# Optimization experiments

Hardware: AMD Instinct MI355X
Metric: run time of the kernel (lower is better)

## Reference

```python
import jax, jax.numpy as jnp
import numpy as np

TAU = 0.1            # tau_instance == tau_proto == tau_guidance
ALPHA_RES = 0.2
LOGIT_SCALE = 5.0
K_NEI = 5
N_WAYS = 20
N_SHOTS = 5


def l2n(x):
    return x / jnp.maximum(jnp.linalg.norm(x, axis=-1, keepdims=True), 1e-12)


def sparse_adj(f, k, tau):
    # sim: [B, n, n]; keep only top-k per row, softmax over them
    sim = jnp.einsum('bnd,bmd->bnm', f, f)
    vals, idx = jax.lax.top_k(sim, k)
    B, n, _ = sim.shape
    mask = jnp.full_like(sim, -jnp.inf)
    bi = jnp.arange(B)[:, None, None]
    ri = jnp.arange(n)[None, :, None]
    mask = mask.at[bi, ri, idx].set(vals)
    return jax.nn.softmax(mask / tau, axis=-1)


def gnn_layer(x, adj, W, b, s):
    # message passing + linear + tanh + scaled residual (dropout=0 / eval)
    msg = jnp.einsum('bnm,bmd->bnd', adj, x)
    upd = jnp.tanh(msg @ W.T + b)
    return x + s * upd


def setup_inputs() -> dict:
    key = jax.random.key(0)
    ks = jax.random.split(key, 10)
    B, N, K, Q, D, L = 256, N_WAYS, N_SHOTS, 75, 512, 4
    NT = N * K + Q
    xav = 1.0 / np.sqrt(D)
    return {
        'V_feat': jax.random.normal(ks[0], (B, NT, D), jnp.float32),
        'P_feat': jax.random.normal(ks[1], (B, N, D), jnp.float32),
        'query_y': jax.random.randint(ks[2], (B, Q), 0, N),
        'igb_W': jax.random.normal(ks[3], (L, D, D), jnp.float32) * xav,
        'igb_b': jnp.zeros((L, D), jnp.float32),
        'igb_scale': jax.random.normal(ks[4], (L,), jnp.float32) * 0.1,
        'pgb_W': jax.random.normal(ks[5], (L, D, D), jnp.float32) * xav,
        'pgb_b': jnp.zeros((L, D), jnp.float32),
        'pgb_scale': jax.random.normal(ks[6], (L,), jnp.float32) * 0.1,
        'alpha': jax.random.uniform(ks[7], (), jnp.float32),
        'beta': jax.random.uniform(ks[8], (), jnp.float32),
    }


def reference(V_feat, P_feat, query_y, igb_W, igb_b, igb_scale,
              pgb_W, pgb_b, pgb_scale, alpha, beta):
    B, NT, D = V_feat.shape
    N, K = N_WAYS, N_SHOTS
    NK = N * K
    Q = NT - NK
    L = igb_W.shape[0]

    V = l2n(V_feat)
    P = l2n(P_feat)
    V0, P0 = V, P

    yl = query_y.reshape(B * Q)
    total = jnp.float32(0.0)
    final_logits = None
    for i in range(L):
        # instance graph branch
        adj_I = sparse_adj(V, K_NEI, TAU)
        V = gnn_layer(V, adj_I, igb_W[i], igb_b[i], igb_scale[i])
        V = l2n((1.0 - ALPHA_RES) * V + ALPHA_RES * V0)
        # prototype graph branch
        adj_P = sparse_adj(P, min(K_NEI, N), TAU)
        P = gnn_layer(P, adj_P, pgb_W[i], pgb_b[i], pgb_scale[i])
        P = l2n((1.0 - ALPHA_RES) * P + ALPHA_RES * P0)
        # visual class centers and adapted prototypes
        VC = l2n(V[:, :NK, :].reshape(B, N, K, D).mean(axis=2))
        Pa = l2n(alpha * P + (1.0 - alpha) * VC)
        # cross-modal softmax guidance
        sims = jnp.einsum('bnd,bmd->bnm', V, Pa)
        soft = jax.nn.softmax(sims / TAU, axis=-1)
        guide = jnp.einsum('bnm,bmd->bnd', soft, Pa)
        V = l2n(beta * V + (1.0 - beta) * guide)
        # per-step logits and CE loss (label_smoothing = 0)
        logits = LOGIT_SCALE * jnp.einsum('bqd,bnd->bqn', V[:, NK:, :], Pa)
        lf = logits.reshape(B * Q, N)
        ce = jnp.mean(jax.nn.logsumexp(lf, axis=-1)
                      - jnp.take_along_axis(lf, yl[:, None], axis=1)[:, 0])
        total = total + ce
        final_logits = logits

    loss = total / L
    pred = jnp.argmax(final_logits.reshape(B * Q, N), axis=-1)
    acc = jnp.mean((pred == yl).astype(jnp.float32))
    return (loss, acc)
```

## Files before the change

kernel.cpp:

```cpp
#include <hip/hip_runtime.h>
#include <math.h>

#define B_EP 256
#define NT 175
#define NWAYS 20
#define KSHOT 5
#define NKS 100
#define NQ 75
#define DIM 512
#define NLAYERS 4
#define TAU_INV 10.0f
#define LOGIT_SCALE 5.0f
#define KNEI 5
#define SIMLD 176
#define STLD2 72
#define PALD 520
#define NVB 700

typedef unsigned int u32;
typedef unsigned short u16;
typedef __attribute__((ext_vector_type(8))) short s16x8;
typedef __attribute__((ext_vector_type(4))) float f32x4;

__device__ __forceinline__ float waveReduceSum(float v) {
#pragma unroll
  for (int off = 32; off >= 1; off >>= 1) v += __shfl_xor(v, off);
  return v;
}

__device__ __forceinline__ u32 pack2bf(float a, float b) {
  u32 ua = __float_as_uint(a), ub = __float_as_uint(b);
  ua = (ua + 0x7FFFu + ((ua >> 16) & 1u)) >> 16;
  ub = (ub + 0x7FFFu + ((ub >> 16) & 1u)) >> 16;
  return ua | (ub << 16);
}

__device__ __forceinline__ u16 pack1bf(float a) {
  u32 ua = __float_as_uint(a);
  return (u16)((ua + 0x7FFFu + ((ua >> 16) & 1u)) >> 16);
}

__device__ __forceinline__ float bflo(u32 u) { return __uint_as_float(u << 16); }
__device__ __forceinline__ float bfhi(u32 u) { return __uint_as_float(u & 0xFFFF0000u); }
__device__ __forceinline__ float bf1(u16 h) { return __uint_as_float((u32)h << 16); }

__device__ __forceinline__ float tanh_fast(float x) {
  float e = __expf(2.f * x);
  return 1.f - 2.f * __builtin_amdgcn_rcpf(e + 1.f);
}

__device__ __forceinline__ s16x8 ldfrag(const u16* p) {
  return __builtin_bit_cast(s16x8, *(const uint4*)p);
}

__device__ __forceinline__ void gload16(const u16* g, u16* l) {
  __builtin_amdgcn_global_load_lds(
      (const __attribute__((address_space(1))) void*)g,
      (__attribute__((address_space(3))) void*)l, 16, 0, 0);
}

__global__ void init_accum_kernel(float* acc) {
  if (threadIdx.x < 16) acc[threadIdx.x] = 0.f;
}

__global__ void cvt_bf16_kernel(const float* __restrict__ in1,
                                const float* __restrict__ in2,
                                u16* __restrict__ outb, int n8_each) {
  const int nb1 = (n8_each + 255) / 256;
  int bid = blockIdx.x;
  const float* in = (bid < nb1) ? in1 : in2;
  u16* out = (bid < nb1) ? outb : outb + (size_t)n8_each * 8;
  if (bid >= nb1) bid -= nb1;
  int t = bid * 256 + threadIdx.x;
  if (t >= n8_each) return;
  const float4* p = (const float4*)(in + (size_t)t * 8);
  float4 a = p[0], b = p[1];
  uint4 r;
  r.x = pack2bf(a.x, a.y);
  r.y = pack2bf(a.z, a.w);
  r.z = pack2bf(b.x, b.y);
  r.w = pack2bf(b.z, b.w);
  *(uint4*)(out + (size_t)t * 8) = r;
}

__global__ void l2n_init_kernel(const float* __restrict__ in,
                                u16* __restrict__ outb,
                                u16* __restrict__ out0b) {
  const size_t row = blockIdx.x;
  const int lane = threadIdx.x;
  const float* src = in + row * DIM;
  float4 a = *(const float4*)(src + 4 * lane);
  float4 b = *(const float4*)(src + 256 + 4 * lane);
  float ss = a.x * a.x + a.y * a.y + a.z * a.z + a.w * a.w +
             b.x * b.x + b.y * b.y + b.z * b.z + b.w * b.w;
  ss = waveReduceSum(ss);
  const float inv = 1.f / fmaxf(sqrtf(ss), 1e-12f);
  a.x *= inv; a.y *= inv; a.z *= inv; a.w *= inv;
  b.x *= inv; b.y *= inv; b.z *= inv; b.w *= inv;
  uint2 pa, pb;
  pa.x = pack2bf(a.x, a.y); pa.y = pack2bf(a.z, a.w);
  pb.x = pack2bf(b.x, b.y); pb.y = pack2bf(b.z, b.w);
  *(uint2*)(outb + row * DIM + 4 * lane) = pa;
  *(uint2*)(outb + row * DIM + 256 + 4 * lane) = pb;
  *(uint2*)(out0b + row * DIM + 4 * lane) = pa;
  *(uint2*)(out0b + row * DIM + 256 + 4 * lane) = pb;
}

__global__ __launch_bounds__(256) void graph_front_kernel(
    const u16* __restrict__ VB, const u16* __restrict__ PB,
    u16* __restrict__ MSGB, u16* __restrict__ PMSGB) {
  const int p = blockIdx.x;
  const int tid = threadIdx.x;
  const int wave = tid >> 6, lane = tid & 63;
  __shared__ __align__(16) u16 smem[25088];
  __shared__ float Gl2[NWAYS][NWAYS];
  __shared__ float Wl2[NWAYS][KNEI];
  __shared__ int Il2[NWAYS][KNEI];
  if (p < 3 * B_EP) {
    const int b = p & 255, sl = p >> 8;
    u16* SIMs = smem;
    u16* Vst = smem + 64 * SIMLD;
    const u16* Vb = VB + (size_t)b * NT * DIM;
    for (int i = tid; i < (192 - NT) * STLD2; i += 256)
      Vst[NT * STLD2 + i] = 0;
    f32x4 acc[4][4];
#pragma unroll
    for (int m = 0; m < 4; ++m)
#pragma unroll
      for (int n = 0; n < 4; ++n) acc[m][n] = (f32x4){0.f, 0.f, 0.f, 0.f};
    const int part = lane >> 4;
    for (int kk = 0; kk < DIM; kk += 64) {
      __syncthreads();
#pragma unroll
      for (int r6 = 0; r6 < 6; ++r6) {
        const int idx = tid + 256 * r6;
        if (idx < NT * 8) {
          const int row = idx >> 3, pp = idx & 7;
          uint4 v = *(const uint4*)(Vb + (size_t)row * DIM + kk + pp * 8);
          *(uint4*)&Vst[row * STLD2 + pp * 8] = v;
        }
      }
      __syncthreads();
      if (wave < 3) {
#pragma unroll
        for (int ks = 0; ks < 2; ++ks) {
          s16x8 fa[4], fb[4];
#pragma unroll
          for (int m = 0; m < 4; ++m)
            fa[m] = ldfrag(&Vst[(sl * 64 + m * 16 + (lane & 15)) * STLD2 +
                                ks * 32 + part * 8]);
#pragma unroll
          for (int n = 0; n < 4; ++n)
            fb[n] = ldfrag(&Vst[(wave * 64 + n * 16 + (lane & 15)) * STLD2 +
                                ks * 32 + part * 8]);
#pragma unroll
          for (int m = 0; m < 4; ++m)
#pragma unroll
            for (int n = 0; n < 4; ++n)
              acc[m][n] = __builtin_amdgcn_mfma_f32_16x16x32_bf16(
                  fa[m], fb[n], acc[m][n], 0, 0, 0);
        }
      }
    }
    const int r_ = (lane >> 4) * 4, c_ = lane & 15;
    if (wave < 3) {
#pragma unroll
      for (int m = 0; m < 4; ++m)
#pragma unroll
        for (int n = 0; n < 4; ++n)
#pragma unroll
          for (int j = 0; j < 4; ++j) {
            const int rl = m * 16 + r_ + j;
            const int c = wave * 64 + n * 16 + c_;
            if (sl * 64 + rl < NT && c < NT)
              SIMs[rl * SIMLD + c] = pack1bf(acc[m][n][j]);
          }
    }
    __syncthreads();
    for (int rl = wave; rl < 64; rl += 4) {
      const int rg = sl * 64 + rl;
      if (rg >= NT) break;
      u32 pk[3];
#pragma unroll
      for (int t = 0; t < 3; ++t) {
        int j = lane + 64 * t;
        if (j < NT) {
          u32 v = SIMs[rl * SIMLD + j];
          u32 key = v ^ ((v >> 15) ? 0xFFFFu : 0x8000u);
          pk[t] = (key << 8) | (u32)(255 - j);
        } else {
          pk[t] = 0u;
        }
      }
      float topv[KNEI];
      int topi[KNEI];
#pragma unroll
      for (int t = 0; t < KNEI; ++t) {
        u32 c = max(pk[0], max(pk[1], pk[2]));
#pragma unroll
        for (int off = 32; off >= 1; off >>= 1)
          c = max(c, (u32)__shfl_xor((int)c, off));
#pragma unroll
        for (int u = 0; u < 3; ++u)
          if (pk[u] == c) pk[u] = 0u;
        const u32 k16 = (c >> 8) & 0xFFFFu;
        const u32 v16 = (k16 & 0x8000u) ? (k16 ^ 0x8000u) : (~k16 & 0xFFFFu);
        topv[t] = bf1((u16)v16);
        topi[t] = 255 - (int)(c & 0xFFu);
      }
      float w[KNEI];
      float wsum = 0.f;
#pragma unroll
      for (int t = 0; t < KNEI; ++t) {
        w[t] = __expf((topv[t] - topv[0]) * TAU_INV);
        wsum += w[t];
      }
      const float invs = 1.f / wsum;
      float a8[8] = {0.f, 0.f, 0.f, 0.f, 0.f, 0.f, 0.f, 0.f};
#pragma unroll
      for (int t = 0; t < KNEI; ++t) {
        uint4 v = *(const uint4*)(Vb + (size_t)topi[t] * DIM + 8 * lane);
        a8[0] += w[t] * bflo(v.x); a8[1] += w[t] * bfhi(v.x);
        a8[2] += w[t] * bflo(v.y); a8[3] += w[t] * bfhi(v.y);
        a8[4] += w[t] * bflo(v.z); a8[5] += w[t] * bfhi(v.z);
        a8[6] += w[t] * bflo(v.w); a8[7] += w[t] * bfhi(v.w);
      }
      uint4 r;
      r.x = pack2bf(a8[0] * invs, a8[1] * invs);
      r.y = pack2bf(a8[2] * invs, a8[3] * invs);
      r.z = pack2bf(a8[4] * invs, a8[5] * invs);
      r.w = pack2bf(a8[6] * invs, a8[7] * invs);
      *(uint4*)(MSGB + ((size_t)b * NT + rg) * DIM + 8 * lane) = r;
    }
  } else {
    const int b = p - 3 * B_EP;
    u16* Pl = smem;
    const u16* Pb = PB + (size_t)b * NWAYS * DIM;
    for (int c = tid; c < 32 * 64; c += 256) {
      int m = c >> 6, ko = (c & 63) * 8;
      uint4 v = {0, 0, 0, 0};
      if (m < NWAYS) v = *(const uint4*)(Pb + (size_t)m * DIM + ko);
      *(uint4*)&Pl[m * PALD + ko] = v;
    }
    __syncthreads();
    if (wave == 0) {
      f32x4 acc[2][2];
#pragma unroll
      for (int m = 0; m < 2; ++m)
#pragma unroll
        for (int n = 0; n < 2; ++n) acc[m][n] = (f32x4){0.f, 0.f, 0.f, 0.f};
      for (int kk = 0; kk < DIM; kk += 32) {
        s16x8 f[2];
#pragma unroll
        for (int m = 0; m < 2; ++m)
          f[m] = ldfrag(&Pl[(m * 16 + (lane & 15)) * PALD + kk +
                            (lane >> 4) * 8]);
#pragma unroll
        for (int m = 0; m < 2; ++m)
#pragma unroll
          for (int n = 0; n < 2; ++n)
            acc[m][n] = __builtin_amdgcn_mfma_f32_16x16x32_bf16(
                f[m], f[n], acc[m][n], 0, 0, 0);
      }
      const int r_ = (lane >> 4) * 4, c_ = lane & 15;
#pragma unroll
      for (int m = 0; m < 2; ++m)
#pragma unroll
        for (int n = 0; n < 2; ++n)
#pragma unroll
          for (int j = 0; j < 4; ++j) {
            int r = m * 16 + r_ + j, c = n * 16 + c_;
            if (r < NWAYS && c < NWAYS) Gl2[r][c] = acc[m][n][j];
          }
    }
    __syncthreads();
    if (tid < NWAYS) {
      float sims[NWAYS];
#pragma unroll
      for (int m = 0; m < NWAYS; ++m) sims[m] = Gl2[tid][m];
      float topv[KNEI];
      int topi[KNEI];
#pragma unroll
      for (int t = 0; t < KNEI; ++t) {
        float bv = -INFINITY;
        int bi = 0;
#pragma unroll
        for (int m = 0; m < NWAYS; ++m)
          if (sims[m] > bv) { bv = sims[m]; bi = m; }
        sims[bi] = -INFINITY;
        topv[t] = bv;
        topi[t] = bi;
      }
      float w[KNEI], wsum = 0.f;
#pragma unroll
      for (int t = 0; t < KNEI; ++t) {
        w[t] = __expf((topv[t] - topv[0]) * TAU_INV);
        wsum += w[t];
      }
      const float invs = 1.f / wsum;
#pragma unroll
      for (int t = 0; t < KNEI; ++t) {
        Wl2[tid][t] = w[t] * invs;
        Il2[tid][t] = topi[t];
      }
    }
    __syncthreads();
    u16* outp = PMSGB + (size_t)b * NWAYS * DIM;
    for (int n = wave; n < NWAYS; n += 4) {
      float a8[8] = {0.f, 0.f, 0.f, 0.f, 0.f, 0.f, 0.f, 0.f};
#pragma unroll
      for (int t = 0; t < KNEI; ++t) {
        const float w = Wl2[n][t];
        uint4 v = *(const uint4*)&Pl[Il2[n][t] * PALD + 8 * lane];
        a8[0] += w * bflo(v.x); a8[1] += w * bfhi(v.x);
        a8[2] += w * bflo(v.y); a8[3] += w * bfhi(v.y);
        a8[4] += w * bflo(v.z); a8[5] += w * bfhi(v.z);
        a8[6] += w * bflo(v.w); a8[7] += w * bfhi(v.w);
      }
      uint4 r;
      r.x = pack2bf(a8[0], a8[1]);
      r.y = pack2bf(a8[2], a8[3]);
      r.z = pack2bf(a8[4], a8[5]);
      r.w = pack2bf(a8[6], a8[7]);
      *(uint4*)(outp + (size_t)n * DIM + 8 * lane) = r;
    }
  }
}

__global__ __launch_bounds__(512) void gemm_fused_kernel(
    const u16* __restrict__ Av, const u16* __restrict__ Ap,
    const u16* __restrict__ Wv, const u16* __restrict__ Wp,
    const float* __restrict__ bias_v, const float* __restrict__ bias_p,
    const float* __restrict__ sv, const float* __restrict__ sp,
    u16* __restrict__ XBv, u16* __restrict__ XBp,
    const u16* __restrict__ X0v, const u16* __restrict__ X0p) {
  const int bid = blockIdx.x;
  const bool isV = bid < NVB;
  const int row0 = (isV ? bid : bid - NVB) * 64;
  const u16* A = isV ? Av : Ap;
  const u16* W = isV ? Wv : Wp;
  const float* bias = isV ? bias_v : bias_p;
  const float* scale_ptr = isV ? sv : sp;
  u16* XB = isV ? XBv : XBp;
  const u16* X0B = isV ? X0v : X0p;
  const int tid = threadIdx.x, wave = tid >> 6, lane = tid & 63;
  __shared__ __align__(16) u16 smem[18432];
  u16* Bs = smem;
  u16* As = smem + 16384;
  f32x4 acc[4][4];
#pragma unroll
  for (int m = 0; m < 4; ++m)
#pragma unroll
    for (int n = 0; n < 4; ++n) acc[m][n] = (f32x4){0.f, 0.f, 0.f, 0.f};
  const int rsrc = lane >> 2;
  const int ksrc = (lane & 3) * 8;
  for (int kk = 0; kk < DIM; kk += 32) {
#pragma unroll
    for (int q = 0; q < 4; ++q) {
      const int t = wave * 4 + q;
      gload16(W + (size_t)(t * 16 + rsrc) * DIM + kk + ksrc, Bs + t * 512);
    }
    if (wave < 4)
      gload16(A + (size_t)(row0 + wave * 16 + rsrc) * DIM + kk + ksrc,
              As + wave * 512);
    __syncthreads();
    s16x8 fa[4], fb[4];
#pragma unroll
    for (int m = 0; m < 4; ++m)
      fa[m] = ldfrag(&As[(m * 16 + (lane & 15)) * 32 + (lane >> 4) * 8]);
#pragma unroll
    for (int n = 0; n < 4; ++n)
      fb[n] = ldfrag(
          &Bs[(wave * 64 + n * 16 + (lane & 15)) * 32 + (lane >> 4) * 8]);
#pragma unroll
    for (int m = 0; m < 4; ++m)
#pragma unroll
      for (int n = 0; n < 4; ++n)
        acc[m][n] = __builtin_amdgcn_mfma_f32_16x16x32_bf16(fa[m], fb[n],
                                                            acc[m][n], 0, 0, 0);
    __syncthreads();
  }
  const float s = *scale_ptr;
  const int rq = lane >> 4, c_ = lane & 15;
  const int prow = tid >> 4, sub = tid & 15;
  const int rq2 = ((prow >> 2) & 3) << 1;
#pragma unroll
  for (int half = 0; half < 2; ++half) {
    __syncthreads();
#pragma unroll
    for (int n = 0; n < 4; ++n) {
      const int col = wave * 64 + n * 16 + c_;
      const float bc = bias[col];
      const int cbase = col >> 3, wof = col & 7;
#pragma unroll
      for (int mm = 0; mm < 2; ++mm) {
        const int m = half * 2 + mm;
#pragma unroll
        for (int j = 0; j < 4; ++j) {
          const int lr = mm * 16 + rq * 4 + j;
          const int cS = cbase ^ (((lr >> 2) & 3) << 1);
          smem[lr * 512 + cS * 8 + wof] =
              pack1bf(s * tanh_fast(acc[m][n][j] + bc));
        }
      }
    }
    __syncthreads();
    const int grow = row0 + half * 32 + prow;
    const u16* xrow = XB + (size_t)grow * DIM;
    const u16* x0row = X0B + (size_t)grow * DIM;
    float ss = 0.f;
#pragma unroll
    for (int i = 0; i < 4; ++i) {
      const int c = sub + 16 * i;
      uint4 xb = *(const uint4*)(xrow + c * 8);
      uint4 x0 = *(const uint4*)(x0row + c * 8);
      uint4 uu = *(const uint4*)&smem[prow * 512 + (c ^ rq2) * 8];
      float t0 = 0.8f * (bflo(xb.x) + bflo(uu.x)) + 0.2f * bflo(x0.x);
      float t1 = 0.8f * (bfhi(xb.x) + bfhi(uu.x)) + 0.2f * bfhi(x0.x);
      float t2 = 0.8f * (bflo(xb.y) + bflo(uu.y)) + 0.2f * bflo(x0.y);
      float t3 = 0.8f * (bfhi(xb.y) + bfhi(uu.y)) + 0.2f * bfhi(x0.y);
      float t4 = 0.8f * (bflo(xb.z) + bflo(uu.z)) + 0.2f * bflo(x0.z);
      float t5 = 0.8f * (bfhi(xb.z) + bfhi(uu.z)) + 0.2f * bfhi(x0.z);
      float t6 = 0.8f * (bflo(xb.w) + bflo(uu.w)) + 0.2f * bflo(x0.w);
      float t7 = 0.8f * (bfhi(xb.w) + bfhi(uu.w)) + 0.2f * bfhi(x0.w);
      ss += t0 * t0 + t1 * t1 + t2 * t2 + t3 * t3 + t4 * t4 + t5 * t5 +
            t6 * t6 + t7 * t7;
      uint4 tp;
      tp.x = pack2bf(t0, t1); tp.y = pack2bf(t2, t3);
      tp.z = pack2bf(t4, t5); tp.w = pack2bf(t6, t7);
      *(uint4*)&smem[prow * 512 + (c ^ rq2) * 8] = tp;
    }
#pragma unroll
    for (int off = 8; off >= 1; off >>= 1) ss += __shfl_xor(ss, off, 16);
    const float inv = 1.f / fmaxf(sqrtf(ss), 1e-12f);
    u16* orow = XB + (size_t)grow * DIM;
#pragma unroll
    for (int i = 0; i < 4; ++i) {
      const int c = sub + 16 * i;
      uint4 tp = *(const uint4*)&smem[prow * 512 + (c ^ rq2) * 8];
      uint4 r;
      r.x = pack2bf(bflo(tp.x) * inv, bfhi(tp.x) * inv);
      r.y = pack2bf(bflo(tp.y) * inv, bfhi(tp.y) * inv);
      r.z = pack2bf(bflo(tp.z) * inv, bfhi(tp.z) * inv);
      r.w = pack2bf(bflo(tp.w) * inv, bfhi(tp.w) * inv);
      *(uint4*)(orow + c * 8) = r;
    }
  }
}

__global__ __launch_bounds__(512) void episode_post_kernel(
    u16* __restrict__ VB, const u16* __restrict__ PB,
    const int* __restrict__ qy, const float* __restrict__ alpha_ptr,
    const float* __restrict__ beta_ptr, float* __restrict__ accum,
    int is_last) {
  const int p = blockIdx.x;
  const int b = p & 255, sl = p >> 8;
  const int tid = threadIdx.x, wave = tid >> 6, lane = tid & 63;
  __shared__ __align__(16) u16 palds[NWAYS * PALD];
  __shared__ float SIMSl[96 * NWAYS];
  __shared__ float Gl[NWAYS][NWAYS + 1];
  __shared__ float red[16];
  const u16* Vb0 = VB + (size_t)b * NT * DIM;
  const float alpha = *alpha_ptr, oma = 1.f - alpha;
  const float beta = *beta_ptr, omb = 1.f - beta;
  const int row_lo = sl * 96;
  const int row_hi = (row_lo + 96 < NT) ? (row_lo + 96) : NT;
  for (int n = wave; n < NWAYS; n += 8) {
    const u16* base = Vb0 + (size_t)n * KSHOT * DIM;
    float a8[8] = {0.f, 0.f, 0.f, 0.f, 0.f, 0.f, 0.f, 0.f};
#pragma unroll
    for (int k = 0; k < KSHOT; ++k) {
      uint4 v = *(const uint4*)(base + (size_t)k * DIM + 8 * lane);
      a8[0] += bflo(v.x); a8[1] += bfhi(v.x);
      a8[2] += bflo(v.y); a8[3] += bfhi(v.y);
      a8[4] += bflo(v.z); a8[5] += bfhi(v.z);
      a8[6] += bflo(v.w); a8[7] += bfhi(v.w);
    }
    float ss = 0.f;
#pragma unroll
    for (int t = 0; t < 8; ++t) ss += a8[t] * a8[t];
    ss = waveReduceSum(ss);
    const float inv = 1.f / fmaxf(sqrtf(ss), 1e-12f);
    {
      uint4 pp = *(const uint4*)(PB + ((size_t)b * NWAYS + n) * DIM + 8 * lane);
      a8[0] = alpha * bflo(pp.x) + oma * a8[0] * inv;
      a8[1] = alpha * bfhi(pp.x) + oma * a8[1] * inv;
      a8[2] = alpha * bflo(pp.y) + oma * a8[2] * inv;
      a8[3] = alpha * bfhi(pp.y) + oma * a8[3] * inv;
      a8[4] = alpha * bflo(pp.z) + oma * a8[4] * inv;
      a8[5] = alpha * bfhi(pp.z) + oma * a8[5] * inv;
      a8[6] = alpha * bflo(pp.w) + oma * a8[6] * inv;
      a8[7] = alpha * bfhi(pp.w) + oma * a8[7] * inv;
    }
    float s2 = 0.f;
#pragma unroll
    for (int t = 0; t < 8; ++t) s2 += a8[t] * a8[t];
    s2 = waveReduceSum(s2);
    const float inv2 = 1.f / fmaxf(sqrtf(s2), 1e-12f);
    uint4 r;
    r.x = pack2bf(a8[0] * inv2, a8[1] * inv2);
    r.y = pack2bf(a8[2] * inv2, a8[3] * inv2);
    r.z = pack2bf(a8[4] * inv2, a8[5] * inv2);
    r.w = pack2bf(a8[6] * inv2, a8[7] * inv2);
    *(uint4*)&palds[n * PALD + 8 * lane] = r;
  }
  __syncthreads();
  if (wave < 4) {
    const int r0w = (wave < 3) ? (row_lo + wave * 32) : NT;
    f32x4 sacc[2][2];
#pragma unroll
    for (int m = 0; m < 2; ++m)
#pragma unroll
      for (int n = 0; n < 2; ++n) sacc[m][n] = (f32x4){0.f, 0.f, 0.f, 0.f};
    const int part = lane >> 4, fr = lane & 15;
    for (int kk = 0; kk < DIM; kk += 32) {
      s16x8 fa[2], fb[2];
#pragma unroll
      for (int m = 0; m < 2; ++m) {
        const int row = r0w + m * 16 + fr;
        if (row < NT) {
          fa[m] = __builtin_bit_cast(
              s16x8, *(const uint4*)(Vb0 + (size_t)row * DIM + kk + part * 8));
        } else {
          int pr = row - NT;
          if (pr > NWAYS - 1) pr = NWAYS - 1;
          fa[m] = ldfrag(&palds[pr * PALD + kk + part * 8]);
        }
      }
#pragma unroll
      for (int n = 0; n < 2; ++n)
        fb[n] = ldfrag(&palds[(n * 16 + fr) * PALD + kk + part * 8]);
#pragma unroll
      for (int m = 0; m < 2; ++m)
#pragma unroll
        for (int n = 0; n < 2; ++n)
          sacc[m][n] = __builtin_amdgcn_mfma_f32_16x16x32_bf16(
              fa[m], fb[n], sacc[m][n], 0, 0, 0);
    }
    const int r_ = (lane >> 4) * 4, c_ = lane & 15;
#pragma unroll
    for (int m = 0; m < 2; ++m)
#pragma unroll
      for (int n = 0; n < 2; ++n)
#pragma unroll
        for (int j = 0; j < 4; ++j) {
          const int r = r0w + m * 16 + r_ + j, c = n * 16 + c_;
          if (c >= NWAYS) continue;
          if (r >= row_lo && r < row_hi && wave < 3)
            SIMSl[(r - row_lo) * NWAYS + c] = sacc[m][n][j];
          else if (r >= NT && r < NT + NWAYS)
            Gl[r - NT][c] = sacc[m][n][j];
        }
  }
  __syncthreads();
  float ce_acc = 0.f, ac_acc = 0.f;
  if (!(is_last && sl == 0)) {
    const int rs = is_last ? ((row_lo > NKS ? row_lo : NKS) + wave)
                           : (row_lo + wave);
    for (int row = rs; row < row_hi; row += 8) {
      float s[NWAYS];
#pragma unroll
      for (int m = 0; m < NWAYS; ++m)
        s[m] = SIMSl[(row - row_lo) * NWAYS + m];
      float mx = s[0];
#pragma unroll
      for (int m = 1; m < NWAYS; ++m) mx = fmaxf(mx, s[m]);
      float e[NWAYS], wsum = 0.f, dN = 0.f;
#pragma unroll
      for (int m = 0; m < NWAYS; ++m) {
        e[m] = __expf((s[m] - mx) * TAU_INV);
        wsum += e[m];
        dN += e[m] * s[m];
      }
      const float cg = omb / wsum;
      const int ln = lane & 31;
      float sg = 0.f;
      if (ln < NWAYS) {
#pragma unroll
        for (int m = 0; m < NWAYS; ++m) sg += e[m] * Gl[m][ln];
      }
      float ege = (ln < NWAYS) ? e[ln] * sg : 0.f;
#pragma unroll
      for (int off = 16; off >= 1; off >>= 1) ege += __shfl_xor(ege, off, 32);
      const float nn2 = beta * beta + 2.f * beta * cg * dN + cg * cg * ege;
      const float inv = 1.f / fmaxf(sqrtf(nn2), 1e-12f);
      if (!is_last) {
        u16* vrow = VB + ((size_t)b * NT + row) * DIM;
        uint4 v4 = *(const uint4*)(vrow + 8 * lane);
        float t0 = 0.f, t1 = 0.f, t2 = 0.f, t3 = 0.f;
        float t4 = 0.f, t5 = 0.f, t6 = 0.f, t7 = 0.f;
#pragma unroll
        for (int m = 0; m < NWAYS; ++m) {
          uint4 pp = *(const uint4*)&palds[m * PALD + 8 * lane];
          t0 += e[m] * bflo(pp.x); t1 += e[m] * bfhi(pp.x);
          t2 += e[m] * bflo(pp.y); t3 += e[m] * bfhi(pp.y);
          t4 += e[m] * bflo(pp.z); t5 += e[m] * bfhi(pp.z);
          t6 += e[m] * bflo(pp.w); t7 += e[m] * bfhi(pp.w);
        }
        uint4 r;
        r.x = pack2bf((beta * bflo(v4.x) + cg * t0) * inv,
                      (beta * bfhi(v4.x) + cg * t1) * inv);
        r.y = pack2bf((beta * bflo(v4.y) + cg * t2) * inv,
                      (beta * bfhi(v4.y) + cg * t3) * inv);
        r.z = pack2bf((beta * bflo(v4.z) + cg * t4) * inv,
                      (beta * bfhi(v4.z) + cg * t5) * inv);
        r.w = pack2bf((beta * bflo(v4.w) + cg * t6) * inv,
                      (beta * bfhi(v4.w) + cg * t7) * inv);
        *(uint4*)(vrow + 8 * lane) = r;
      }
      if (row >= NKS) {
        float l = (ln < NWAYS)
                      ? LOGIT_SCALE * inv * (beta * s[ln] + cg * sg)
                      : -1e30f;
        float bv = l;
        int bi = ln;
#pragma unroll
        for (int off = 16; off >= 1; off >>= 1) {
          float ov = __shfl_xor(bv, off, 32);
          int oi = __shfl_xor(bi, off, 32);
          if (ov > bv || (ov == bv && oi < bi)) { bv = ov; bi = oi; }
        }
        float se = (ln < NWAYS) ? __expf(l - bv) : 0.f;
#pragma unroll
        for (int off = 16; off >= 1; off >>= 1) se += __shfl_xor(se, off, 32);
        const int yt = qy[b * NQ + (row - NKS)];
        const float ly = __shfl(l, yt, 32);
        if (lane == 0) {
          ce_acc += bv + __logf(se) - ly;
          ac_acc += (bi == yt) ? 1.f : 0.f;
        }
      }
    }
  }
  if (lane == 0) {
    red[wave] = ce_acc;
    red[8 + wave] = ac_acc;
  }
  __syncthreads();
  if (tid == 0 && sl == 1) {
    float ce = 0.f, ac = 0.f;
#pragma unroll
    for (int w8 = 0; w8 < 8; ++w8) {
      ce += red[w8];
      ac += red[8 + w8];
    }
    atomicAdd(&accum[0], ce);
    if (is_last) atomicAdd(&accum[1], ac);
  } else if (tid == 0 && sl == 0 && !is_last) {
    float ce = 0.f;
#pragma unroll
    for (int w8 = 0; w8 < 8; ++w8) ce += red[w8];
    atomicAdd(&accum[0], ce);
  }
}

__global__ void finalize_kernel(const float* __restrict__ acc,
                                float* __restrict__ out) {
  out[0] = acc[0] / (float)(NLAYERS * B_EP * NQ);
  out[1] = acc[1] / (float)(B_EP * NQ);
}

extern "C" void kernel_launch(void* const* d_in, const int* in_sizes, int n_in,
                              void* d_out, int out_size, void* d_ws,
                              size_t ws_size, hipStream_t stream) {
  const float* V_feat = (const float*)d_in[0];
  const float* P_feat = (const float*)d_in[1];
  const int* query_y = (const int*)d_in[2];
  const float* igb_W = (const float*)d_in[3];
  const float* igb_b = (const float*)d_in[4];
  const float* igb_s = (const float*)d_in[5];
  const float* pgb_W = (const float*)d_in[6];
  const float* pgb_b = (const float*)d_in[7];
  const float* pgb_s = (const float*)d_in[8];
  const float* alpha = (const float*)d_in[9];
  const float* beta = (const float*)d_in[10];
  float* out = (float*)d_out;

  float* ws = (float*)d_ws;
  const size_t vsz = (size_t)B_EP * NT * DIM;
  const size_t psz = (size_t)B_EP * NWAYS * DIM;
  const size_t wsz = (size_t)NLAYERS * DIM * DIM;
  float* ACC = ws;
  u16* VB = (u16*)(ws + 16);
  u16* V0B = VB + vsz;
  u16* MSGB = V0B + vsz;
  u16* PB = MSGB + vsz;
  u16* P0B = PB + psz;
  u16* PMSGB = P0B + psz;
  u16* WB = PMSGB + psz;
  u16* WPB = WB + wsz;

  init_accum_kernel<<<1, 64, 0, stream>>>(ACC);
  l2n_init_kernel<<<B_EP * NT, 64, 0, stream>>>(V_feat, VB, V0B);
  l2n_init_kernel<<<B_EP * NWAYS, 64, 0, stream>>>(P_feat, PB, P0B);
  {
    const int n8 = (int)(wsz / 8);
    const int nb1 = (n8 + 255) / 256;
    cvt_bf16_kernel<<<2 * nb1, 256, 0, stream>>>(igb_W, pgb_W, WB, n8);
  }

  for (int i = 0; i < NLAYERS; ++i) {
    graph_front_kernel<<<4 * B_EP, 256, 0, stream>>>(VB, PB, MSGB, PMSGB);
    gemm_fused_kernel<<<NVB + B_EP * NWAYS / 64, 512, 0, stream>>>(
        MSGB, PMSGB, WB + (size_t)i * DIM * DIM, WPB + (size_t)i * DIM * DIM,
        igb_b + (size_t)i * DIM, pgb_b + (size_t)i * DIM, igb_s + i, pgb_s + i,
        VB, PB, V0B, P0B);
    episode_post_kernel<<<2 * B_EP, 512, 0, stream>>>(
        VB, PB, query_y, alpha, beta, ACC, (i == NLAYERS - 1) ? 1 : 0);
  }
  finalize_kernel<<<1, 1, 0, stream>>>(ACC, out);
}
```

Baseline: 768.5 us.

## Compute guidance update soft@Pa with MFMA using split-bf16 weights

```diff
diff --git a/kernel.cpp b/kernel.cpp
--- a/kernel.cpp
+++ b/kernel.cpp
@@ -15,6 +15,8 @@
 #define SIMLD 176
 #define STLD2 72
 #define PALD 520
+#define PTLD 32
+#define ELD 64
 #define NVB 700
 
 typedef unsigned int u32;
@@ -457,14 +459,18 @@
   const int b = p & 255, sl = p >> 8;
   const int tid = threadIdx.x, wave = tid >> 6, lane = tid & 63;
   __shared__ __align__(16) u16 palds[NWAYS * PALD];
+  __shared__ __align__(16) u16 PaT[512 * PTLD];
+  __shared__ __align__(16) u16 El[96 * ELD];
   __shared__ float SIMSl[96 * NWAYS];
   __shared__ float Gl[NWAYS][NWAYS + 1];
+  __shared__ float rowscal[96][2];
   __shared__ float red[16];
   const u16* Vb0 = VB + (size_t)b * NT * DIM;
   const float alpha = *alpha_ptr, oma = 1.f - alpha;
   const float beta = *beta_ptr, omb = 1.f - beta;
   const int row_lo = sl * 96;
   const int row_hi = (row_lo + 96 < NT) ? (row_lo + 96) : NT;
+  const int nrows = row_hi - row_lo;
   for (int n = wave; n < NWAYS; n += 8) {
     const u16* base = Vb0 + (size_t)n * KSHOT * DIM;
     float a8[8] = {0.f, 0.f, 0.f, 0.f, 0.f, 0.f, 0.f, 0.f};
@@ -497,12 +503,24 @@
     for (int t = 0; t < 8; ++t) s2 += a8[t] * a8[t];
     s2 = waveReduceSum(s2);
     const float inv2 = 1.f / fmaxf(sqrtf(s2), 1e-12f);
+    u16 h[8];
+#pragma unroll
+    for (int t = 0; t < 8; ++t) h[t] = pack1bf(a8[t] * inv2);
     uint4 r;
-    r.x = pack2bf(a8[0] * inv2, a8[1] * inv2);
-    r.y = pack2bf(a8[2] * inv2, a8[3] * inv2);
-    r.z = pack2bf(a8[4] * inv2, a8[5] * inv2);
-    r.w = pack2bf(a8[6] * inv2, a8[7] * inv2);
+    r.x = (u32)h[0] | ((u32)h[1] << 16);
+    r.y = (u32)h[2] | ((u32)h[3] << 16);
+    r.z = (u32)h[4] | ((u32)h[5] << 16);
+    r.w = (u32)h[6] | ((u32)h[7] << 16);
     *(uint4*)&palds[n * PALD + 8 * lane] = r;
+    if (!is_last) {
+#pragma unroll
+      for (int t = 0; t < 8; ++t)
+        PaT[(8 * lane + t) * PTLD + n] = h[t];
+    }
+  }
+  if (!is_last) {
+#pragma unroll
+    for (int z = 0; z < 12; ++z) PaT[tid * PTLD + NWAYS + z] = 0;
   }
   __syncthreads();
   if (wave < 4) {
@@ -552,6 +570,10 @@
             Gl[r - NT][c] = sacc[m][n][j];
         }
   }
+  if (!is_last) {
+    for (int i = tid; i < (96 - nrows) * ELD; i += 512)
+      El[nrows * ELD + i] = 0;
+  }
   __syncthreads();
   float ce_acc = 0.f, ac_acc = 0.f;
   if (!(is_last && sl == 0)) {
@@ -585,28 +607,17 @@
       const float nn2 = beta * beta + 2.f * beta * cg * dN + cg * cg * ege;
       const float inv = 1.f / fmaxf(sqrtf(nn2), 1e-12f);
       if (!is_last) {
-        u16* vrow = VB + ((size_t)b * NT + row) * DIM;
-        uint4 v4 = *(const uint4*)(vrow + 8 * lane);
-        float t0 = 0.f, t1 = 0.f, t2 = 0.f, t3 = 0.f;
-        float t4 = 0.f, t5 = 0.f, t6 = 0.f, t7 = 0.f;
-#pragma unroll
-        for (int m = 0; m < NWAYS; ++m) {
-          uint4 pp = *(const uint4*)&palds[m * PALD + 8 * lane];
-          t0 += e[m] * bflo(pp.x); t1 += e[m] * bfhi(pp.x);
-          t2 += e[m] * bflo(pp.y); t3 += e[m] * bfhi(pp.y);
-          t4 += e[m] * bflo(pp.z); t5 += e[m] * bfhi(pp.z);
-          t6 += e[m] * bflo(pp.w); t7 += e[m] * bfhi(pp.w);
-        }
-        uint4 r;
-        r.x = pack2bf((beta * bflo(v4.x) + cg * t0) * inv,
-                      (beta * bfhi(v4.x) + cg * t1) * inv);
-        r.y = pack2bf((beta * bflo(v4.y) + cg * t2) * inv,
-                      (beta * bfhi(v4.y) + cg * t3) * inv);
-        r.z = pack2bf((beta * bflo(v4.z) + cg * t4) * inv,
-                      (beta * bfhi(v4.z) + cg * t5) * inv);
-        r.w = pack2bf((beta * bflo(v4.w) + cg * t6) * inv,
-                      (beta * bfhi(v4.w) + cg * t7) * inv);
-        *(uint4*)(vrow + 8 * lane) = r;
+        u16 hi = 0, lo = 0;
+        if (ln < NWAYS) {
+          hi = pack1bf(e[ln]);
+          lo = pack1bf(e[ln] - bf1(hi));
+        }
+        El[(row - row_lo) * ELD + ln] = hi;
+        El[(row - row_lo) * ELD + 32 + ln] = lo;
+        if (lane == 0) {
+          rowscal[row - row_lo][0] = beta * inv;
+          rowscal[row - row_lo][1] = cg * inv;
+        }
       }
       if (row >= NKS) {
         float l = (ln < NWAYS)
@@ -637,6 +648,33 @@
     red[8 + wave] = ac_acc;
   }
   __syncthreads();
+  if (!is_last) {
+    const int tr = row_lo + wave * 16;
+    if (tr < row_hi) {
+      const int fr = lane & 15, part = lane >> 4;
+      const int er = (tr - row_lo + fr) * ELD + part * 8;
+      const s16x8 fahi = ldfrag(&El[er]);
+      const s16x8 falo = ldfrag(&El[er + 32]);
+      u16* vb = VB + ((size_t)b * NT) * DIM;
+      for (int t = 0; t < 32; ++t) {
+        const s16x8 fb = ldfrag(&PaT[(t * 16 + fr) * PTLD + part * 8]);
+        f32x4 acc = (f32x4){0.f, 0.f, 0.f, 0.f};
+        acc = __builtin_amdgcn_mfma_f32_16x16x32_bf16(fahi, fb, acc, 0, 0, 0);
+        acc = __builtin_amdgcn_mfma_f32_16x16x32_bf16(falo, fb, acc, 0, 0, 0);
+        const int gc = t * 16 + fr;
+#pragma unroll
+        for (int j = 0; j < 4; ++j) {
+          const int gr = tr + part * 4 + j;
+          if (gr < row_hi) {
+            const float bi_ = rowscal[gr - row_lo][0];
+            const float cgi = rowscal[gr - row_lo][1];
+            u16* vp = vb + (size_t)gr * DIM + gc;
+            *vp = pack1bf(bi_ * bf1(*vp) + cgi * acc[j]);
+          }
+        }
+      }
+    }
+  }
   if (tid == 0 && sl == 1) {
     float ce = 0.f, ac = 0.f;
 #pragma unroll
```

New measurement: 818.8 us. +6.6%, slower.
